# Kernel optimization log

Hardware: AMD Instinct MI355X
Metric: run time of the kernel (lower is better)

The kernel has to match this reference:

```python
import jax, jax.numpy as jnp
import numpy as np

H = 12  # num_attention_heads


def setup_inputs() -> dict:
    key = jax.random.key(0)
    ks = jax.random.split(key, 7)
    B, T, L, D = 4, 64, 128, 768
    input_ids = jax.random.randint(ks[0], (B, T, L), 0, 30000, dtype=jnp.int32)
    speaker_ids = jax.random.randint(ks[1], (B, T), 0, 8, dtype=jnp.int32)
    token_embeddings = jax.random.normal(ks[2], (B, T, L, D), dtype=jnp.float32)
    edu_embeddings = jax.random.normal(ks[3], (B, T, D), dtype=jnp.float32)
    s = 1.0 / np.sqrt(D)
    Wk = jax.random.normal(ks[4], (D, D), dtype=jnp.float32) * s
    Wv = jax.random.normal(ks[5], (D, D), dtype=jnp.float32) * s
    Wq = jax.random.normal(ks[6], (D, D), dtype=jnp.float32) * s
    return {"input_ids": input_ids, "speaker_ids": speaker_ids,
            "token_embeddings": token_embeddings, "edu_embeddings": edu_embeddings,
            "Wk": Wk, "Wv": Wv, "Wq": Wq}


def reference(input_ids, speaker_ids, token_embeddings, edu_embeddings, Wk, Wv, Wq):
    B, T, L = input_ids.shape
    D = token_embeddings.shape[-1]
    d = D // H
    # per-turn keys/values, split into heads: [B,T,H,d]
    k = (edu_embeddings @ Wk.T).reshape(B, T, H, d)
    v = (edu_embeddings @ Wv.T).reshape(B, T, H, d)
    # per-head outer products k (x) v: [B,T,H,d,d]
    kv = jnp.einsum('bthd,bthe->bthde', k, v)
    # speaker-segmented inclusive prefix sum: M[b,t] = sum_{u<=t, spk[u]==spk[t]} kv[b,u]
    same = speaker_ids[:, None, :] == speaker_ids[:, :, None]        # [B,T(t),T(u)]
    causal = jnp.tril(jnp.ones((T, T), dtype=bool))                  # u <= t (inclusive)
    A = (same & causal).astype(kv.dtype)                             # [B,T,T]
    M = jnp.einsum('btu,buhde->bthde', A, kv)                        # [B,T,H,d,d]
    # token queries attend into their turn's speaker memory matrix
    q = (token_embeddings @ Wq.T).reshape(B, T, L, H, d)
    a = jnp.einsum('btlhd,bthde->btlhe', q, M).reshape(B, T, L, D)
    return token_embeddings + a
```

## Files before the change

### kernel.cpp

```cpp
#include <hip/hip_runtime.h>
#include <hip/hip_bf16.h>

#define NB 4
#define NT 64
#define NL 128
#define ND 768
#define NH 12
#define HD 64

typedef __attribute__((ext_vector_type(8))) short short8;
typedef __attribute__((ext_vector_type(4))) float f32x4;
typedef __attribute__((ext_vector_type(4))) unsigned int u32x4;

typedef __attribute__((address_space(3))) unsigned int lds_u32;
typedef __attribute__((address_space(1))) const unsigned int glob_u32;

static __device__ __forceinline__ unsigned short f2b(float x) {
    __hip_bfloat16 h = __float2bfloat16(x);
    return *reinterpret_cast<unsigned short*>(&h);
}
static __device__ __forceinline__ float b2f(unsigned short u) {
    unsigned int v = ((unsigned int)u) << 16;
    union { unsigned int i; float f; } c; c.i = v; return c.f;
}
static __device__ __forceinline__ void gl2lds16(const void* g, void* l) {
    __builtin_amdgcn_global_load_lds((glob_u32*)g, (lds_u32*)l, 16, 0, 0);
}
static __device__ __forceinline__ unsigned rne2(unsigned lo, unsigned hi) {
    lo += 0x7FFFu + ((lo >> 16) & 1u);
    hi += 0x7FFFu + ((hi >> 16) & 1u);
    return __builtin_amdgcn_perm(hi, lo, 0x07060302u);
}

__global__ __launch_bounds__(256) void prep_all(
    const float* __restrict__ te, const float* __restrict__ Wq,
    const float* __restrict__ edu, const float* __restrict__ Wk,
    const float* __restrict__ Wv, const int* __restrict__ spk,
    unsigned short* __restrict__ te_b, unsigned short* __restrict__ wq_b,
    unsigned short* __restrict__ Mt)
{
    __shared__ __align__(16) unsigned char sm[113920];
    const int tid = threadIdx.x;
    const unsigned bid = blockIdx.x;

    if (bid >= 96u) {
        if (bid < 3168u) {
            const unsigned base = (bid - 96u) * 2048u + tid;
            u32x4 a[8];
            #pragma unroll
            for (int i = 0; i < 8; i++)
                a[i] = __builtin_nontemporal_load((const u32x4*)te + base + i * 256u);
            #pragma unroll
            for (int i = 0; i < 8; i++) {
                uint2 o;
                o.x = rne2(a[i].x, a[i].y);
                o.y = rne2(a[i].z, a[i].w);
                *(uint2*)(te_b + (size_t)(base + i * 256u) * 4u) = o;
            }
        } else {
            const unsigned base = (bid - 3168u) * 2048u + tid;
            u32x4 a[8];
            #pragma unroll
            for (int i = 0; i < 8; i++)
                a[i] = *((const u32x4*)Wq + base + i * 256u);
            #pragma unroll
            for (int i = 0; i < 8; i++) {
                uint2 o;
                o.x = rne2(a[i].x, a[i].y);
                o.y = rne2(a[i].z, a[i].w);
                *(uint2*)(wq_b + (size_t)(base + i * 256u) * 4u) = o;
            }
        }
        return;
    }

    const int h  = bid % 12;
    const int b  = (bid / 12) & 3;
    const int eh = bid / 48;

    float (*bucket)[32][65]  = (float (*)[32][65])(sm);
    float (*k_s)[68]         = (float (*)[68])(sm + 66560);
    float (*v_s)[36]         = (float (*)[36])(sm + 83968);
    unsigned short* edu_s    = (unsigned short*)(sm + 93184);
    unsigned short* wk_s     = edu_s + 4096;
    unsigned short* wv_s     = edu_s + 8192;
    int* spk_s               = (int*)(sm + 113664);

    const int lane = tid & 63, wvx = tid >> 6;
    const int lr = lane & 15, lg = lane >> 4;

    { float* p = &bucket[0][0][0];
      for (int i = tid; i < 8 * 32 * 65; i += 256) p[i] = 0.f; }
    if (tid < 64) spk_s[tid] = spk[b * NT + tid];

    const float* eduf = edu + (size_t)(b * 64) * ND;
    const float* wkf  = Wk  + (size_t)(h * 64) * ND;
    const float* wvf  = Wv  + (size_t)(h * 64 + eh * 32) * ND;

    f32x4 acc_k[4], acc_v[2];
    #pragma unroll
    for (int i = 0; i < 4; i++) acc_k[i] = (f32x4){0.f, 0.f, 0.f, 0.f};
    #pragma unroll
    for (int i = 0; i < 2; i++) acc_v[i] = (f32x4){0.f, 0.f, 0.f, 0.f};

    for (int k0 = 0; k0 < ND; k0 += 64) {
        __syncthreads();
        #pragma unroll
        for (int i = 0; i < 2; i++) {
            const int g = tid * 2 + i, row = g >> 3, ch = g & 7;
            const u32x4* p = (const u32x4*)(eduf + (size_t)row * ND + k0 + ch * 8);
            u32x4 x = p[0], y = p[1];
            u32x4 o = { rne2(x.x, x.y), rne2(x.z, x.w), rne2(y.x, y.y), rne2(y.z, y.w) };
            *(u32x4*)&edu_s[row * 64 + ((ch ^ (row & 7)) * 8)] = o;
        }
        #pragma unroll
        for (int i = 0; i < 2; i++) {
            const int g = tid * 2 + i, row = g >> 3, ch = g & 7;
            const u32x4* p = (const u32x4*)(wkf + (size_t)row * ND + k0 + ch * 8);
            u32x4 x = p[0], y = p[1];
            u32x4 o = { rne2(x.x, x.y), rne2(x.z, x.w), rne2(y.x, y.y), rne2(y.z, y.w) };
            *(u32x4*)&wk_s[row * 64 + ((ch ^ (row & 7)) * 8)] = o;
        }
        {
            const int g = tid, row = g >> 3, ch = g & 7;
            const u32x4* p = (const u32x4*)(wvf + (size_t)row * ND + k0 + ch * 8);
            u32x4 x = p[0], y = p[1];
            u32x4 o = { rne2(x.x, x.y), rne2(x.z, x.w), rne2(y.x, y.y), rne2(y.z, y.w) };
            *(u32x4*)&wv_s[row * 64 + ((ch ^ (row & 7)) * 8)] = o;
        }
        __syncthreads();
        #pragma unroll
        for (int k32 = 0; k32 < 2; k32++) {
            const int cx = (((k32 * 4 + lg) ^ (lr & 7)) * 8);
            short8 eb = *(const short8*)&edu_s[(wvx * 16 + lr) * 64 + cx];
            #pragma unroll
            for (int jb = 0; jb < 4; jb++) {
                short8 ak = *(const short8*)&wk_s[(jb * 16 + lr) * 64 + cx];
                acc_k[jb] = __builtin_amdgcn_mfma_f32_16x16x32_bf16(ak, eb, acc_k[jb], 0, 0, 0);
            }
            #pragma unroll
            for (int jb = 0; jb < 2; jb++) {
                short8 av = *(const short8*)&wv_s[(jb * 16 + lr) * 64 + cx];
                acc_v[jb] = __builtin_amdgcn_mfma_f32_16x16x32_bf16(av, eb, acc_v[jb], 0, 0, 0);
            }
        }
    }

    {
        const int t = wvx * 16 + lr;
        #pragma unroll
        for (int jb = 0; jb < 4; jb++) *(f32x4*)&k_s[t][jb * 16 + lg * 4] = acc_k[jb];
        #pragma unroll
        for (int jb = 0; jb < 2; jb++) *(f32x4*)&v_s[t][jb * 16 + lg * 4] = acc_v[jb];
    }
    __syncthreads();

    const int e = tid & 31, dg = tid >> 5;
    for (int t = 0; t < NT; t++) {
        const int s = spk_s[t];
        const float vv = v_s[t][e];
        unsigned short tmp[8];
        #pragma unroll
        for (int jj = 0; jj < 8; jj++) {
            float m = bucket[s][e][dg * 8 + jj] + k_s[t][dg * 8 + jj] * vv;
            bucket[s][e][dg * 8 + jj] = m;
            tmp[jj] = f2b(m);
        }
        unsigned short* mpp = Mt + (((size_t)(b * NT + t) * NH + h) * HD + eh * 32 + e) * HD + dg * 8;
        *(short8*)mpp = *(short8*)tmp;
    }
}

__global__ __launch_bounds__(256, 2) void fused_qm(
    const unsigned short* __restrict__ te_b,
    const unsigned short* __restrict__ wq_b,
    const unsigned short* __restrict__ Mt,
    float* __restrict__ out)
{
    const int orig = blockIdx.x;
    const int id   = (orig & 7) * 192 + (orig >> 3);
    const int hp   = id % 6;
    const int bt   = id / 6;

    __shared__ __align__(16) unsigned short smem[32768];
    unsigned short* te0 = smem;
    unsigned short* te1 = smem + 8192;
    unsigned short* wq0 = smem + 16384;
    unsigned short* wq1 = smem + 24576;
    unsigned short* q_s = smem;

    const int tid  = threadIdx.x;
    const int lane = tid & 63;
    const int wvx  = tid >> 6;
    const int lr   = lane & 15;
    const int lg   = lane >> 4;
    const int wm   = wvx >> 1;
    const int wn   = wvx & 1;
    const int r8   = lane >> 3;
    const int l8   = lane & 7;
    const int sswz = (l8 ^ r8) * 8;

    const unsigned short* teb = te_b + (size_t)bt * NL * ND;
    const unsigned short* wqb = wq_b + (size_t)hp * 128 * ND;

    f32x4 acc[4][4];
    #pragma unroll
    for (int i = 0; i < 4; i++)
        #pragma unroll
        for (int j = 0; j < 4; j++) acc[i][j] = (f32x4){0.f, 0.f, 0.f, 0.f};

    auto STAGE = [&](unsigned short* tebuf, unsigned short* wqbuf, int k0) {
        #pragma unroll
        for (int j = 0; j < 4; j++) {
            const int rbase = wvx * 32 + j * 8;
            gl2lds16(teb + (size_t)(rbase + r8) * ND + k0 + sswz, tebuf + rbase * 64);
            gl2lds16(wqb + (size_t)(rbase + r8) * ND + k0 + sswz, wqbuf + rbase * 64);
        }
    };
    auto COMPUTE = [&](const unsigned short* tes, const unsigned short* wqs) {
        #pragma unroll
        for (int k32 = 0; k32 < 2; k32++) {
            const int cx = (((k32 * 4 + lg) ^ (lr & 7)) * 8);
            short8 af[4], bfv[4];
            #pragma unroll
            for (int tm = 0; tm < 4; tm++)
                af[tm] = *(const short8*)&wqs[(wm * 64 + tm * 16 + lr) * 64 + cx];
            #pragma unroll
            for (int tn = 0; tn < 4; tn++)
                bfv[tn] = *(const short8*)&tes[(wn * 64 + tn * 16 + lr) * 64 + cx];
            #pragma unroll
            for (int tm = 0; tm < 4; tm++)
                #pragma unroll
                for (int tn = 0; tn < 4; tn++)
                    acc[tm][tn] = __builtin_amdgcn_mfma_f32_16x16x32_bf16(
                        af[tm], bfv[tn], acc[tm][tn], 0, 0, 0);
        }
    };

    STAGE(te0, wq0, 0);
    asm volatile("s_waitcnt vmcnt(0)" ::: "memory");
    __builtin_amdgcn_sched_barrier(0);
    __builtin_amdgcn_s_barrier();

    #pragma unroll
    for (int kt = 0; kt < 12; kt += 2) {
        STAGE(te1, wq1, (kt + 1) * 64);
        asm volatile("s_waitcnt vmcnt(8)" ::: "memory");
        __builtin_amdgcn_sched_barrier(0);
        __builtin_amdgcn_s_barrier();
        COMPUTE(te0, wq0);
        asm volatile("s_waitcnt lgkmcnt(0)" ::: "memory");
        __builtin_amdgcn_s_barrier();
        if (kt + 2 < 12) {
            STAGE(te0, wq0, (kt + 2) * 64);
            asm volatile("s_waitcnt vmcnt(8)" ::: "memory");
        } else {
            asm volatile("s_waitcnt vmcnt(0)" ::: "memory");
        }
        __builtin_amdgcn_sched_barrier(0);
        __builtin_amdgcn_s_barrier();
        COMPUTE(te1, wq1);
        asm volatile("s_waitcnt lgkmcnt(0)" ::: "memory");
        __builtin_amdgcn_s_barrier();
    }

    #pragma unroll
    for (int tm = 0; tm < 4; tm++) {
        const int d0 = wm * 64 + tm * 16 + lg * 4;
        #pragma unroll
        for (int tn = 0; tn < 4; tn++) {
            const int ltok = wn * 64 + tn * 16 + lr;
            f32x4 a = acc[tm][tn];
            uint2 w2;
            w2.x = (unsigned)f2b(a.x) | ((unsigned)f2b(a.y) << 16);
            w2.y = (unsigned)f2b(a.z) | ((unsigned)f2b(a.w) << 16);
            *(uint2*)&q_s[ltok * 136 + d0] = w2;
        }
    }

    const int h2 = wvx & 1;
    const int lh = wvx >> 1;
    const unsigned short* mp = Mt + ((size_t)(bt * NH) + hp * 2 + h2) * (HD * HD);
    short8 bfr[8];
    #pragma unroll
    for (int tn = 0; tn < 4; tn++)
        #pragma unroll
        for (int k32 = 0; k32 < 2; k32++)
            bfr[tn * 2 + k32] =
                *(const short8*)&mp[(tn * 16 + lr) * 64 + k32 * 32 + lg * 8];
    __syncthreads();

    f32x4 acc2[4][4];
    #pragma unroll
    for (int i = 0; i < 4; i++)
        #pragma unroll
        for (int j = 0; j < 4; j++) acc2[i][j] = (f32x4){0.f, 0.f, 0.f, 0.f};

    #pragma unroll
    for (int k32 = 0; k32 < 2; k32++) {
        const int ko = k32 * 32 + lg * 8;
        short8 af[4];
        #pragma unroll
        for (int tm = 0; tm < 4; tm++)
            af[tm] = *(const short8*)&q_s[(lh * 64 + tm * 16 + lr) * 136 + h2 * 64 + ko];
        #pragma unroll
        for (int tm = 0; tm < 4; tm++)
            #pragma unroll
            for (int tn = 0; tn < 4; tn++)
                acc2[tm][tn] = __builtin_amdgcn_mfma_f32_16x16x32_bf16(
                    af[tm], bfr[tn * 2 + k32], acc2[tm][tn], 0, 0, 0);
    }

    float* ob = out + (size_t)bt * NL * ND;
    #pragma unroll
    for (int tm = 0; tm < 4; tm++) {
        const int l0 = lh * 64 + tm * 16 + lg * 4;
        #pragma unroll
        for (int tn = 0; tn < 4; tn++) {
            const int cg = hp * 128 + h2 * 64 + tn * 16 + lr;
            f32x4 a = acc2[tm][tn];
            #pragma unroll
            for (int r = 0; r < 4; r++) {
                size_t gi = (size_t)(l0 + r) * ND + cg;
                ob[gi] = b2f(teb[gi]) + a[r];
            }
        }
    }
}

extern "C" void kernel_launch(void* const* d_in, const int* in_sizes, int n_in,
                              void* d_out, int out_size, void* d_ws, size_t ws_size,
                              hipStream_t stream)
{
    const int*   spk = (const int*)d_in[1];
    const float* te  = (const float*)d_in[2];
    const float* edu = (const float*)d_in[3];
    const float* Wk  = (const float*)d_in[4];
    const float* Wv  = (const float*)d_in[5];
    const float* Wq  = (const float*)d_in[6];
    float* out = (float*)d_out;

    unsigned short* bf    = (unsigned short*)d_ws;
    unsigned short* te_bb = bf;
    unsigned short* wq_bb = bf + 25165824u;
    unsigned short* Mtbuf = bf + 25755648u;

    prep_all<<<3240, 256, 0, stream>>>(te, Wq, edu, Wk, Wv, spk,
                                       te_bb, wq_bb, Mtbuf);
    fused_qm<<<6 * NT * NB, 256, 0, stream>>>(te_bb, wq_bb, Mtbuf, out);
}
```

Before: 101.8 us.

## Keep per-speaker memory accumulators in registers and shrink prep LDS footprint

The speaker-segmented prefix sum in prep_all no longer keeps an 8x32x65 float bucket array in LDS. Each wave now owns two speakers and holds their running d×e accumulators in registers, scanning all turns and skipping turns of other speakers. The k_s/v_s staging buffers alias the bf16 operand tiles, so LDS drops from about 111KB to about 26KB, which allows more blocks per CU and removes the bucket zero-fill. The cost is 32 float registers per lane, a serial scan over all turns in every wave, and load imbalance when speakers are unevenly distributed.

```diff
diff --git a/kernel.cpp b/kernel.cpp
--- a/kernel.cpp
+++ b/kernel.cpp
@@ -22,6 +22,9 @@
 static __device__ __forceinline__ float b2f(unsigned short u) {
     unsigned int v = ((unsigned int)u) << 16;
     union { unsigned int i; float f; } c; c.i = v; return c.f;
+}
+static __device__ __forceinline__ unsigned fbits(float f) {
+    union { float f; unsigned u; } c; c.f = f; return c.u;
 }
 static __device__ __forceinline__ void gl2lds16(const void* g, void* l) {
     __builtin_amdgcn_global_load_lds((glob_u32*)g, (lds_u32*)l, 16, 0, 0);
@@ -39,7 +42,7 @@
     unsigned short* __restrict__ te_b, unsigned short* __restrict__ wq_b,
     unsigned short* __restrict__ Mt)
 {
-    __shared__ __align__(16) unsigned char sm[113920];
+    __shared__ __align__(16) unsigned char sm[26880];
     const int tid = threadIdx.x;
     const unsigned bid = blockIdx.x;
 
@@ -78,19 +81,16 @@
     const int b  = (bid / 12) & 3;
     const int eh = bid / 48;
 
-    float (*bucket)[32][65]  = (float (*)[32][65])(sm);
-    float (*k_s)[68]         = (float (*)[68])(sm + 66560);
-    float (*v_s)[36]         = (float (*)[36])(sm + 83968);
-    unsigned short* edu_s    = (unsigned short*)(sm + 93184);
-    unsigned short* wk_s     = edu_s + 4096;
-    unsigned short* wv_s     = edu_s + 8192;
-    int* spk_s               = (int*)(sm + 113664);
+    unsigned short* edu_s = (unsigned short*)(sm);
+    unsigned short* wk_s  = (unsigned short*)(sm + 8192);
+    unsigned short* wv_s  = (unsigned short*)(sm + 16384);
+    float (*k_s)[68]      = (float (*)[68])(sm);
+    float (*v_s)[36]      = (float (*)[36])(sm + 17408);
+    int* spk_s            = (int*)(sm + 26624);
 
     const int lane = tid & 63, wvx = tid >> 6;
     const int lr = lane & 15, lg = lane >> 4;
 
-    { float* p = &bucket[0][0][0];
-      for (int i = tid; i < 8 * 32 * 65; i += 256) p[i] = 0.f; }
     if (tid < 64) spk_s[tid] = spk[b * NT + tid];
 
     const float* eduf = edu + (size_t)(b * 64) * ND;
@@ -146,6 +146,7 @@
         }
     }
 
+    __syncthreads();
     {
         const int t = wvx * 16 + lr;
         #pragma unroll
@@ -155,19 +156,31 @@
     }
     __syncthreads();
 
-    const int e = tid & 31, dg = tid >> 5;
-    for (int t = 0; t < NT; t++) {
-        const int s = spk_s[t];
-        const float vv = v_s[t][e];
-        unsigned short tmp[8];
-        #pragma unroll
-        for (int jj = 0; jj < 8; jj++) {
-            float m = bucket[s][e][dg * 8 + jj] + k_s[t][dg * 8 + jj] * vv;
-            bucket[s][e][dg * 8 + jj] = m;
-            tmp[jj] = f2b(m);
-        }
-        unsigned short* mpp = Mt + (((size_t)(b * NT + t) * NH + h) * HD + eh * 32 + e) * HD + dg * 8;
-        *(short8*)mpp = *(short8*)tmp;
+    const int e  = lane & 31;
+    const int dh = lane >> 5;
+    #pragma unroll
+    for (int sp = 0; sp < 2; sp++) {
+        const int s = wvx + sp * 4;
+        float bk[32];
+        #pragma unroll
+        for (int j = 0; j < 32; j++) bk[j] = 0.f;
+        for (int t = 0; t < NT; t++) {
+            if (spk_s[t] != s) continue;
+            const float vv = v_s[t][e];
+            unsigned short* mpp = Mt +
+                (((size_t)(b * NT + t) * NH + h) * HD + eh * 32 + e) * HD + dh * 32;
+            #pragma unroll
+            for (int q = 0; q < 4; q++) {
+                #pragma unroll
+                for (int j = 0; j < 8; j++)
+                    bk[q * 8 + j] += k_s[t][dh * 32 + q * 8 + j] * vv;
+                u32x4 o = { rne2(fbits(bk[q * 8 + 0]), fbits(bk[q * 8 + 1])),
+                            rne2(fbits(bk[q * 8 + 2]), fbits(bk[q * 8 + 3])),
+                            rne2(fbits(bk[q * 8 + 4]), fbits(bk[q * 8 + 5])),
+                            rne2(fbits(bk[q * 8 + 6]), fbits(bk[q * 8 + 7])) };
+                *(u32x4*)(mpp + q * 8) = o;
+            }
+        }
     }
 }
 
```

Result: no change. 103.7 us (+1.9%).

## Load Wq fragments straight into registers and shrink LDS for higher occupancy

Applied to the files above, without the earlier changes.

The Wq operand of the Q projection GEMM is now loaded from global memory directly into double-buffered registers instead of being staged through LDS. Only the token-embedding tiles stay in LDS, so shared memory shrinks to about 34 KB and launch bounds ask for 3 blocks per CU. This removes the LDS writes and reads for Wq and is meant to raise occupancy. The cost is 16 extra short8 registers per thread under a tighter register budget, possible spills, and uncoalesced global reads of Wq. The vmcnt waits are retuned for the new count of outstanding loads.

```diff
diff --git a/kernel.cpp b/kernel.cpp
--- a/kernel.cpp
+++ b/kernel.cpp
@@ -171,7 +171,7 @@
     }
 }
 
-__global__ __launch_bounds__(256, 2) void fused_qm(
+__global__ __launch_bounds__(256, 3) void fused_qm(
     const unsigned short* __restrict__ te_b,
     const unsigned short* __restrict__ wq_b,
     const unsigned short* __restrict__ Mt,
@@ -182,11 +182,9 @@
     const int hp   = id % 6;
     const int bt   = id / 6;
 
-    __shared__ __align__(16) unsigned short smem[32768];
+    __shared__ __align__(16) unsigned short smem[17408];
     unsigned short* te0 = smem;
     unsigned short* te1 = smem + 8192;
-    unsigned short* wq0 = smem + 16384;
-    unsigned short* wq1 = smem + 24576;
     unsigned short* q_s = smem;
 
     const int tid  = threadIdx.x;
@@ -209,22 +207,28 @@
         #pragma unroll
         for (int j = 0; j < 4; j++) acc[i][j] = (f32x4){0.f, 0.f, 0.f, 0.f};
 
-    auto STAGE = [&](unsigned short* tebuf, unsigned short* wqbuf, int k0) {
+    short8 wqrA[8], wqrB[8];
+
+    auto STAGE_TE = [&](unsigned short* tebuf, int k0) {
         #pragma unroll
         for (int j = 0; j < 4; j++) {
             const int rbase = wvx * 32 + j * 8;
             gl2lds16(teb + (size_t)(rbase + r8) * ND + k0 + sswz, tebuf + rbase * 64);
-            gl2lds16(wqb + (size_t)(rbase + r8) * ND + k0 + sswz, wqbuf + rbase * 64);
         }
     };
-    auto COMPUTE = [&](const unsigned short* tes, const unsigned short* wqs) {
+    auto LOADWQ = [&](short8 (&dst)[8], int k0) {
+        #pragma unroll
+        for (int tm = 0; tm < 4; tm++)
+            #pragma unroll
+            for (int k32 = 0; k32 < 2; k32++)
+                dst[tm * 2 + k32] = *(const short8*)&wqb[
+                    (size_t)(wm * 64 + tm * 16 + lr) * ND + k0 + k32 * 32 + lg * 8];
+    };
+    auto COMPUTE = [&](const unsigned short* tes, const short8 (&wqr)[8]) {
         #pragma unroll
         for (int k32 = 0; k32 < 2; k32++) {
             const int cx = (((k32 * 4 + lg) ^ (lr & 7)) * 8);
-            short8 af[4], bfv[4];
-            #pragma unroll
-            for (int tm = 0; tm < 4; tm++)
-                af[tm] = *(const short8*)&wqs[(wm * 64 + tm * 16 + lr) * 64 + cx];
+            short8 bfv[4];
             #pragma unroll
             for (int tn = 0; tn < 4; tn++)
                 bfv[tn] = *(const short8*)&tes[(wn * 64 + tn * 16 + lr) * 64 + cx];
@@ -233,33 +237,33 @@
                 #pragma unroll
                 for (int tn = 0; tn < 4; tn++)
                     acc[tm][tn] = __builtin_amdgcn_mfma_f32_16x16x32_bf16(
-                        af[tm], bfv[tn], acc[tm][tn], 0, 0, 0);
+                        wqr[tm * 2 + k32], bfv[tn], acc[tm][tn], 0, 0, 0);
         }
     };
 
-    STAGE(te0, wq0, 0);
-    asm volatile("s_waitcnt vmcnt(0)" ::: "memory");
-    __builtin_amdgcn_sched_barrier(0);
-    __builtin_amdgcn_s_barrier();
+    LOADWQ(wqrA, 0);
+    STAGE_TE(te0, 0);
 
     #pragma unroll
     for (int kt = 0; kt < 12; kt += 2) {
-        STAGE(te1, wq1, (kt + 1) * 64);
-        asm volatile("s_waitcnt vmcnt(8)" ::: "memory");
+        LOADWQ(wqrB, (kt + 1) * 64);
+        STAGE_TE(te1, (kt + 1) * 64);
+        asm volatile("s_waitcnt vmcnt(12)" ::: "memory");
         __builtin_amdgcn_sched_barrier(0);
         __builtin_amdgcn_s_barrier();
-        COMPUTE(te0, wq0);
+        COMPUTE(te0, wqrA);
         asm volatile("s_waitcnt lgkmcnt(0)" ::: "memory");
         __builtin_amdgcn_s_barrier();
         if (kt + 2 < 12) {
-            STAGE(te0, wq0, (kt + 2) * 64);
-            asm volatile("s_waitcnt vmcnt(8)" ::: "memory");
+            LOADWQ(wqrA, (kt + 2) * 64);
+            STAGE_TE(te0, (kt + 2) * 64);
+            asm volatile("s_waitcnt vmcnt(12)" ::: "memory");
         } else {
             asm volatile("s_waitcnt vmcnt(0)" ::: "memory");
         }
         __builtin_amdgcn_sched_barrier(0);
         __builtin_amdgcn_s_barrier();
-        COMPUTE(te1, wq1);
+        COMPUTE(te1, wqrB);
         asm volatile("s_waitcnt lgkmcnt(0)" ::: "memory");
         __builtin_amdgcn_s_barrier();
     }
```

Result: slower. 142.2 us (+39.7%).

## Split M-prep blocks along key dimension and alias LDS to cut shared memory

Applied to the files above, without the earlier changes.

The K/V projection and speaker-segmented prefix-sum blocks are split further, across the d half as well as the e half, doubling the block count from 96 to 192 and halving each block's bucket and K tile. Shared memory per block shrinks from about 114KB to about 52KB by aliasing the staging tiles with the bucket, which now gets zeroed after the GEMM loop. This should give more blocks per CU and more parallelism in the serial 64-step scan. The cost is that the edu and Wv tiles are loaded and converted twice.

```diff
diff --git a/kernel.cpp b/kernel.cpp
--- a/kernel.cpp
+++ b/kernel.cpp
@@ -22,6 +22,9 @@
 static __device__ __forceinline__ float b2f(unsigned short u) {
     unsigned int v = ((unsigned int)u) << 16;
     union { unsigned int i; float f; } c; c.i = v; return c.f;
+}
+static __device__ __forceinline__ unsigned fbits(float f) {
+    union { float f; unsigned u; } c; c.f = f; return c.u;
 }
 static __device__ __forceinline__ void gl2lds16(const void* g, void* l) {
     __builtin_amdgcn_global_load_lds((glob_u32*)g, (lds_u32*)l, 16, 0, 0);
@@ -39,13 +42,13 @@
     unsigned short* __restrict__ te_b, unsigned short* __restrict__ wq_b,
     unsigned short* __restrict__ Mt)
 {
-    __shared__ __align__(16) unsigned char sm[113920];
+    __shared__ __align__(16) unsigned char sm[52480];
     const int tid = threadIdx.x;
     const unsigned bid = blockIdx.x;
 
-    if (bid >= 96u) {
-        if (bid < 3168u) {
-            const unsigned base = (bid - 96u) * 2048u + tid;
+    if (bid >= 192u) {
+        if (bid < 3264u) {
+            const unsigned base = (bid - 192u) * 2048u + tid;
             u32x4 a[8];
             #pragma unroll
             for (int i = 0; i < 8; i++)
@@ -58,7 +61,7 @@
                 *(uint2*)(te_b + (size_t)(base + i * 256u) * 4u) = o;
             }
         } else {
-            const unsigned base = (bid - 3168u) * 2048u + tid;
+            const unsigned base = (bid - 3264u) * 2048u + tid;
             u32x4 a[8];
             #pragma unroll
             for (int i = 0; i < 8; i++)
@@ -74,32 +77,33 @@
         return;
     }
 
-    const int h  = bid % 12;
-    const int b  = (bid / 12) & 3;
-    const int eh = bid / 48;
-
-    float (*bucket)[32][65]  = (float (*)[32][65])(sm);
-    float (*k_s)[68]         = (float (*)[68])(sm + 66560);
-    float (*v_s)[36]         = (float (*)[36])(sm + 83968);
-    unsigned short* edu_s    = (unsigned short*)(sm + 93184);
-    unsigned short* wk_s     = edu_s + 4096;
-    unsigned short* wv_s     = edu_s + 8192;
-    int* spk_s               = (int*)(sm + 113664);
+    const int q   = bid / 48;
+    const int rem = bid % 48;
+    const int h   = rem % 12;
+    const int b   = rem / 12;
+    const int eh  = q >> 1;
+    const int dhh = q & 1;
+
+    float (*bucket)[32][33] = (float (*)[32][33])(sm);
+    float (*k_s)[36]        = (float (*)[36])(sm + 33792);
+    float (*v_s)[36]        = (float (*)[36])(sm + 43008);
+    int* spk_s              = (int*)(sm + 52224);
+    unsigned short* edu_s   = (unsigned short*)(sm);
+    unsigned short* wk_s    = (unsigned short*)(sm + 8192);
+    unsigned short* wv_s    = (unsigned short*)(sm + 12288);
 
     const int lane = tid & 63, wvx = tid >> 6;
     const int lr = lane & 15, lg = lane >> 4;
 
-    { float* p = &bucket[0][0][0];
-      for (int i = tid; i < 8 * 32 * 65; i += 256) p[i] = 0.f; }
     if (tid < 64) spk_s[tid] = spk[b * NT + tid];
 
     const float* eduf = edu + (size_t)(b * 64) * ND;
-    const float* wkf  = Wk  + (size_t)(h * 64) * ND;
+    const float* wkf  = Wk  + (size_t)(h * 64 + dhh * 32) * ND;
     const float* wvf  = Wv  + (size_t)(h * 64 + eh * 32) * ND;
 
-    f32x4 acc_k[4], acc_v[2];
-    #pragma unroll
-    for (int i = 0; i < 4; i++) acc_k[i] = (f32x4){0.f, 0.f, 0.f, 0.f};
+    f32x4 acc_k[2], acc_v[2];
+    #pragma unroll
+    for (int i = 0; i < 2; i++) acc_k[i] = (f32x4){0.f, 0.f, 0.f, 0.f};
     #pragma unroll
     for (int i = 0; i < 2; i++) acc_v[i] = (f32x4){0.f, 0.f, 0.f, 0.f};
 
@@ -113,9 +117,8 @@
             u32x4 o = { rne2(x.x, x.y), rne2(x.z, x.w), rne2(y.x, y.y), rne2(y.z, y.w) };
             *(u32x4*)&edu_s[row * 64 + ((ch ^ (row & 7)) * 8)] = o;
         }
-        #pragma unroll
-        for (int i = 0; i < 2; i++) {
-            const int g = tid * 2 + i, row = g >> 3, ch = g & 7;
+        {
+            const int g = tid, row = g >> 3, ch = g & 7;
             const u32x4* p = (const u32x4*)(wkf + (size_t)row * ND + k0 + ch * 8);
             u32x4 x = p[0], y = p[1];
             u32x4 o = { rne2(x.x, x.y), rne2(x.z, x.w), rne2(y.x, y.y), rne2(y.z, y.w) };
@@ -134,7 +137,7 @@
             const int cx = (((k32 * 4 + lg) ^ (lr & 7)) * 8);
             short8 eb = *(const short8*)&edu_s[(wvx * 16 + lr) * 64 + cx];
             #pragma unroll
-            for (int jb = 0; jb < 4; jb++) {
+            for (int jb = 0; jb < 2; jb++) {
                 short8 ak = *(const short8*)&wk_s[(jb * 16 + lr) * 64 + cx];
                 acc_k[jb] = __builtin_amdgcn_mfma_f32_16x16x32_bf16(ak, eb, acc_k[jb], 0, 0, 0);
             }
@@ -146,10 +149,13 @@
         }
     }
 
+    __syncthreads();
+    { float* p = &bucket[0][0][0];
+      for (int i = tid; i < 8 * 32 * 33; i += 256) p[i] = 0.f; }
     {
         const int t = wvx * 16 + lr;
         #pragma unroll
-        for (int jb = 0; jb < 4; jb++) *(f32x4*)&k_s[t][jb * 16 + lg * 4] = acc_k[jb];
+        for (int jb = 0; jb < 2; jb++) *(f32x4*)&k_s[t][jb * 16 + lg * 4] = acc_k[jb];
         #pragma unroll
         for (int jb = 0; jb < 2; jb++) *(f32x4*)&v_s[t][jb * 16 + lg * 4] = acc_v[jb];
     }
@@ -159,15 +165,20 @@
     for (int t = 0; t < NT; t++) {
         const int s = spk_s[t];
         const float vv = v_s[t][e];
-        unsigned short tmp[8];
-        #pragma unroll
-        for (int jj = 0; jj < 8; jj++) {
-            float m = bucket[s][e][dg * 8 + jj] + k_s[t][dg * 8 + jj] * vv;
-            bucket[s][e][dg * 8 + jj] = m;
-            tmp[jj] = f2b(m);
-        }
-        unsigned short* mpp = Mt + (((size_t)(b * NT + t) * NH + h) * HD + eh * 32 + e) * HD + dg * 8;
-        *(short8*)mpp = *(short8*)tmp;
+        float m0 = bucket[s][e][dg * 4 + 0] + k_s[t][dg * 4 + 0] * vv;
+        float m1 = bucket[s][e][dg * 4 + 1] + k_s[t][dg * 4 + 1] * vv;
+        float m2 = bucket[s][e][dg * 4 + 2] + k_s[t][dg * 4 + 2] * vv;
+        float m3 = bucket[s][e][dg * 4 + 3] + k_s[t][dg * 4 + 3] * vv;
+        bucket[s][e][dg * 4 + 0] = m0;
+        bucket[s][e][dg * 4 + 1] = m1;
+        bucket[s][e][dg * 4 + 2] = m2;
+        bucket[s][e][dg * 4 + 3] = m3;
+        uint2 o;
+        o.x = rne2(fbits(m0), fbits(m1));
+        o.y = rne2(fbits(m2), fbits(m3));
+        unsigned short* mpp = Mt +
+            (((size_t)(b * NT + t) * NH + h) * HD + eh * 32 + e) * HD + dhh * 32 + dg * 4;
+        *(uint2*)mpp = o;
     }
 }
 
@@ -345,7 +356,7 @@
     unsigned short* wq_bb = bf + 25165824u;
     unsigned short* Mtbuf = bf + 25755648u;
 
-    prep_all<<<3240, 256, 0, stream>>>(te, Wq, edu, Wk, Wv, spk,
+    prep_all<<<3336, 256, 0, stream>>>(te, Wq, edu, Wk, Wv, spk,
                                        te_bb, wq_bb, Mtbuf);
     fused_qm<<<6 * NT * NB, 256, 0, stream>>>(te_bb, wq_bb, Mtbuf, out);
 }
```

Result: faster. 96.29 us (-5.4%).
